# Optimization experiments

Measured on AMD Instinct MI355X. Metric: run time of the kernel, lower is better.

## Reference

```python
import jax, jax.numpy as jnp
import numpy as np

BATCH, SEQ, STATE, OBS, INP = 4096, 512, 16, 8, 4


def setup_inputs() -> dict:
    key = jax.random.key(0)
    ks = jax.random.split(key, 5)
    # scale A to spectral radius ~0.3 so the 512-step recursion is stable
    A = jax.random.normal(ks[0], (STATE, STATE), jnp.float32) * (0.3 / np.sqrt(STATE))
    B = jax.random.normal(ks[1], (STATE, INP), jnp.float32) * 0.1
    C = jax.random.normal(ks[2], (OBS, STATE), jnp.float32) * (1.0 / np.sqrt(STATE))
    Q = jnp.eye(STATE, dtype=jnp.float32)   # module default when Q is None
    R = jnp.eye(OBS, dtype=jnp.float32)     # module default when R is None
    x0 = jnp.zeros((STATE,), jnp.float32)   # module default initial_state_mean
    obs = jax.random.normal(ks[3], (BATCH, SEQ, OBS), jnp.float32)
    u = jax.random.normal(ks[4], (BATCH, SEQ, INP), jnp.float32)
    return {"obs": obs, "u": u, "A": A, "B": B, "C": C, "Q": Q, "R": R, "x0": x0}


def reference(obs, u, A, B, C, Q, R, x0):
    Bsz = obs.shape[0]
    S = A.shape[0]
    eyeS = jnp.eye(S, dtype=obs.dtype)
    x_init = jnp.broadcast_to(x0, (Bsz, S))                 # (B,S), P0 = I per module init
    P_init = jnp.broadcast_to(eyeS, (Bsz, S, S))

    def step(carry, inp):
        x, P = carry                                        # x:(B,S)  P:(B,S,S)
        u_k, z_k = inp                                      # (B,I), (B,O)
        # stage 1: prediction
        x_prior = x @ A.T + u_k @ B.T                       # (B,S)
        P_prior = A @ P @ A.T + Q                           # (B,S,S)
        # stage 2: measurement update
        Smat = C @ P_prior @ C.T + R                        # (B,O,O) innovation covariance
        K = P_prior @ C.T @ jnp.linalg.inv(Smat)            # (B,S,O)
        innov = z_k - x_prior @ C.T                         # (B,O)
        x_post = x_prior + jnp.einsum('bso,bo->bs', K, innov)
        P_post = (eyeS - K @ C) @ P_prior                   # (B,S,S)
        return (x_post, P_post), x_post

    inp_seq = (jnp.swapaxes(u, 0, 1), jnp.swapaxes(obs, 0, 1))  # time-major for scan
    _, xs = jax.lax.scan(step, (x_init, P_init), inp_seq)       # xs: (T,B,S)
    return jnp.swapaxes(xs, 0, 1)                               # (B,T,S) == states_est[:,1:,:]
```

## Files before the change

### kernel.cpp

```cpp
#include <hip/hip_runtime.h>
#include <hip/hip_bf16.h>

#define SEQ   512
#define BATCH 4096
#define NS    16
#define NO    8
#define NI    4
#define NK    12
#define CH    32
#define CL    (SEQ/CH)
#define CW    16

__device__ __align__(16) float g_gains[NK * 448];
__device__ int   g_isf32_data;
__device__ float g_x0[NS];

static __device__ __forceinline__ float bf2f_us(unsigned short v) {
    unsigned int u = ((unsigned int)v) << 16;
    return __uint_as_float(u);
}

static __device__ __forceinline__ float4 ld4(const float* p) { return *(const float4*)p; }
static __device__ __forceinline__ void st4(float* p, float4 v) { *(float4*)p = v; }
static __device__ __forceinline__ void fma4(float4& a, float s, float4 b) {
    a.x += s*b.x; a.y += s*b.y; a.z += s*b.z; a.w += s*b.w;
}
static __device__ __forceinline__ void fnma4(float4& a, float s, float4 b) {
    a.x -= s*b.x; a.y -= s*b.y; a.z -= s*b.z; a.w -= s*b.w;
}

__global__ __launch_bounds__(64) void riccati_kernel(
        const void* __restrict__ Ap, const void* __restrict__ Bp,
        const void* __restrict__ Cp, const void* __restrict__ Qp,
        const void* __restrict__ Rp, const void* __restrict__ x0p,
        const void* __restrict__ obsp) {
    __shared__ __align__(16) float A[NS*NS], AT[NS*NS], Q[NS*NS];
    __shared__ __align__(16) float P[NS*NS], AP[NS*NS], Pp[NS*NS];
    __shared__ __align__(16) float Cm[NO*NS], CT[NS*NO], Bm[NS*NI], R[NO*NO];
    __shared__ __align__(16) float CA[NO*NS], CB[NO*NI];
    __shared__ __align__(16) float CP[NO*NS], PCt[NS*NO], K[NS*NO];
    __shared__ __align__(16) float G[NO*2*NO];
    __shared__ int sflag_p, sflag_d;

    const int t  = threadIdx.x;
    const int i  = t >> 2;
    const int jq = t & 3;
    const int j0 = jq * 4;

    if (t == 0) { sflag_p = 0; sflag_d = 0; }
    __syncthreads();
    {
        const unsigned short* ah = (const unsigned short*)Ap;
        for (int s = 0; s < 4; ++s) {
            float v = fabsf(bf2f_us(ah[t + 64*s]));
            if (!(v < 16.0f)) sflag_p = 1;
        }
        const unsigned short* oh = (const unsigned short*)obsp;
        for (int s = 0; s < 32; ++s) {
            float w = fabsf(bf2f_us(oh[t + 64*s]));
            if (!(w < 16.0f)) sflag_d = 1;
        }
    }
    __syncthreads();
    const bool f32p = (sflag_p != 0);
    if (t == 0) g_isf32_data = (sflag_d != 0) ? 1 : 0;

    auto ld = [&](const void* p, int idx) -> float {
        return f32p ? ((const float*)p)[idx]
                    : bf2f_us(((const unsigned short*)p)[idx]);
    };

    for (int q = t; q < NS*NS; q += 64) {
        A[q] = ld(Ap, q);
        Q[q] = ld(Qp, q);
        P[q] = ((q >> 4) == (q & 15)) ? 1.0f : 0.0f;
    }
    Bm[t] = ld(Bp, t);
    for (int q = t; q < NO*NS; q += 64) Cm[q] = ld(Cp, q);
    R[t] = ld(Rp, t);
    if (t < NS) g_x0[t] = ld(x0p, t);
    __syncthreads();

    for (int q = t; q < NS*NS; q += 64) AT[(q & 15)*NS + (q >> 4)] = A[q];
    for (int q = t; q < NO*NS; q += 64) CT[(q & 15)*NO + (q >> 4)] = Cm[q];
    if (t < 32) {
        const int io = t >> 2;
        float4 acc = make_float4(0.f, 0.f, 0.f, 0.f);
        for (int l = 0; l < NS; ++l) fma4(acc, Cm[io*NS + l], ld4(&A[l*NS + j0]));
        st4(&CA[io*NS + j0], acc);
    } else if (t < 40) {
        const int io = t - 32;
        float4 acc = make_float4(0.f, 0.f, 0.f, 0.f);
        for (int l = 0; l < NS; ++l) fma4(acc, Cm[io*NS + l], ld4(&Bm[l*NI]));
        st4(&CB[io*NI], acc);
    }
    __syncthreads();

    for (int k = 0; k < NK; ++k) {
        {
            float4 acc = make_float4(0.f, 0.f, 0.f, 0.f);
            for (int l = 0; l < NS; ++l) fma4(acc, A[i*NS + l], ld4(&P[l*NS + j0]));
            st4(&AP[i*NS + j0], acc);
        }
        __syncthreads();
        {
            float4 acc = ld4(&Q[i*NS + j0]);
            for (int l = 0; l < NS; ++l) fma4(acc, AP[i*NS + l], ld4(&AT[l*NS + j0]));
            st4(&Pp[i*NS + j0], acc);
        }
        __syncthreads();
        if (t < 32) {
            const int io = t >> 2;
            float4 acc = make_float4(0.f, 0.f, 0.f, 0.f);
            for (int l = 0; l < NS; ++l) fma4(acc, Cm[io*NS + l], ld4(&Pp[l*NS + j0]));
            st4(&CP[io*NS + j0], acc);
        } else {
            const int t2 = t - 32;
            const int i2 = t2 >> 1, jb = (t2 & 1) * 4;
            float4 acc = make_float4(0.f, 0.f, 0.f, 0.f);
            for (int l = 0; l < NS; ++l) fma4(acc, Pp[i2*NS + l], ld4(&CT[l*NO + jb]));
            st4(&PCt[i2*NO + jb], acc);
        }
        __syncthreads();
        if (t < 32) {
            const int io = t >> 2;
            if (jq < 2) {
                float4 acc = ld4(&R[io*NO + j0]);
                for (int l = 0; l < NS; ++l) fma4(acc, CP[io*NS + l], ld4(&CT[l*NO + j0]));
                st4(&G[io*2*NO + j0], acc);
            } else {
                float4 v = make_float4((j0 + 0 - NO) == io ? 1.f : 0.f,
                                       (j0 + 1 - NO) == io ? 1.f : 0.f,
                                       (j0 + 2 - NO) == io ? 1.f : 0.f,
                                       (j0 + 3 - NO) == io ? 1.f : 0.f);
                st4(&G[io*2*NO + j0], v);
            }
        }
        __syncthreads();
        for (int p = 0; p < NO; ++p) {
            float piv = 1.f, gip = 0.f;
            float4 gp4 = make_float4(0.f, 0.f, 0.f, 0.f);
            float4 g4  = make_float4(0.f, 0.f, 0.f, 0.f);
            if (t < 32) {
                const int io = t >> 2;
                piv = G[p*2*NO + p];
                gip = G[io*2*NO + p];
                gp4 = ld4(&G[p*2*NO + j0]);
                g4  = ld4(&G[io*2*NO + j0]);
            }
            __syncthreads();
            if (t < 32) {
                const int io = t >> 2;
                const float inv = 1.0f / piv;
                float4 r4 = make_float4(gp4.x*inv, gp4.y*inv, gp4.z*inv, gp4.w*inv);
                float4 w;
                if (io == p) w = r4;
                else w = make_float4(g4.x - gip*r4.x, g4.y - gip*r4.y,
                                     g4.z - gip*r4.z, g4.w - gip*r4.w);
                st4(&G[io*2*NO + j0], w);
            }
            __syncthreads();
        }
        if (t < 32) {
            const int i2 = t >> 1, jb = (t & 1) * 4;
            float4 acc = make_float4(0.f, 0.f, 0.f, 0.f);
            for (int l = 0; l < NO; ++l) fma4(acc, PCt[i2*NO + l], ld4(&G[l*2*NO + NO + jb]));
            st4(&K[i2*NO + jb], acc);
        }
        __syncthreads();
        float* outp = g_gains + k * 448;
        {
            float4 m4 = ld4(&A[i*NS + j0]);
            float4 pn = ld4(&Pp[i*NS + j0]);
            for (int l = 0; l < NO; ++l) {
                const float kk = K[i*NO + l];
                fnma4(m4, kk, ld4(&CA[l*NS + j0]));
                fnma4(pn, kk, ld4(&CP[l*NS + j0]));
            }
            st4(outp + i*NS + j0, m4);
            st4(&P[i*NS + j0], pn);
        }
        if (jq == 0) {
            float4 n4 = ld4(&Bm[i*NI]);
            for (int l = 0; l < NO; ++l) fnma4(n4, K[i*NO + l], ld4(&CB[l*NI]));
            st4(outp + 256 + i*NI, n4);
        } else if (jq < 3) {
            const int jb = (jq - 1) * 4;
            st4(outp + 320 + i*NO + jb, ld4(&K[i*NO + jb]));
        }
        __syncthreads();
    }
}

template<bool F32>
static __device__ __forceinline__ void run_filter(
        const void* __restrict__ obsv, const void* __restrict__ uv,
        float* __restrict__ out, int c, int b, const float* __restrict__ sg) {
    const int cL = c * CL;
    const int k0 = (c == 0) ? 0 : (cL - CW);
    const int kend = cL + CL;

    float x[NS];
#pragma unroll
    for (int s = 0; s < NS; ++s) x[s] = (c == 0) ? g_x0[s] : 0.0f;
    float xp[NS];

    float* op = out + (size_t)b * SEQ * NS;

    const float*          upf = (const float*)uv   + (size_t)b * SEQ * NI;
    const float*          zpf = (const float*)obsv + (size_t)b * SEQ * NO;
    const unsigned short* upb = (const unsigned short*)uv   + (size_t)b * SEQ * NI;
    const unsigned short* zpb = (const unsigned short*)obsv + (size_t)b * SEQ * NO;

    float4 uf, zf0, zf1;
    uint2 ub; uint4 zb;
    if (F32) {
        uf  = *(const float4*)(upf + (size_t)k0 * NI);
        zf0 = *(const float4*)(zpf + (size_t)k0 * NO);
        zf1 = *(const float4*)(zpf + (size_t)k0 * NO + 4);
    } else {
        ub = *(const uint2*)(upb + (size_t)k0 * NI);
        zb = *(const uint4*)(zpb + (size_t)k0 * NO);
    }

    for (int k = k0; k < kend; ++k) {
        float uu[NI], zz[NO];
        if (F32) {
            uu[0]=uf.x; uu[1]=uf.y; uu[2]=uf.z; uu[3]=uf.w;
            zz[0]=zf0.x; zz[1]=zf0.y; zz[2]=zf0.z; zz[3]=zf0.w;
            zz[4]=zf1.x; zz[5]=zf1.y; zz[6]=zf1.z; zz[7]=zf1.w;
            if (k + 1 < kend) {
                uf  = *(const float4*)(upf + (size_t)(k+1) * NI);
                zf0 = *(const float4*)(zpf + (size_t)(k+1) * NO);
                zf1 = *(const float4*)(zpf + (size_t)(k+1) * NO + 4);
            }
        } else {
            const uint2 uc = ub; const uint4 zc = zb;
            if (k + 1 < kend) {
                ub = *(const uint2*)(upb + (size_t)(k+1) * NI);
                zb = *(const uint4*)(zpb + (size_t)(k+1) * NO);
            }
            uu[0] = bf2f_us(uc.x & 0xffffu); uu[1] = bf2f_us(uc.x >> 16);
            uu[2] = bf2f_us(uc.y & 0xffffu); uu[3] = bf2f_us(uc.y >> 16);
            zz[0] = bf2f_us(zc.x & 0xffffu); zz[1] = bf2f_us(zc.x >> 16);
            zz[2] = bf2f_us(zc.y & 0xffffu); zz[3] = bf2f_us(zc.y >> 16);
            zz[4] = bf2f_us(zc.z & 0xffffu); zz[5] = bf2f_us(zc.z >> 16);
            zz[6] = bf2f_us(zc.w & 0xffffu); zz[7] = bf2f_us(zc.w >> 16);
        }

        const int idx = (k < NK) ? k : (NK - 1);
        const float4* G = (const float4*)sg + idx * 112;

        float xn[NS];
#pragma unroll
        for (int r = 0; r < NS; ++r) {
            float4 m0 = G[r*4 + 0], m1 = G[r*4 + 1], m2 = G[r*4 + 2], m3 = G[r*4 + 3];
            float acc;
            acc  = m0.x*x[0]  + m0.y*x[1]  + m0.z*x[2]  + m0.w*x[3];
            acc += m1.x*x[4]  + m1.y*x[5]  + m1.z*x[6]  + m1.w*x[7];
            acc += m2.x*x[8]  + m2.y*x[9]  + m2.z*x[10] + m2.w*x[11];
            acc += m3.x*x[12] + m3.y*x[13] + m3.z*x[14] + m3.w*x[15];
            float4 nv = G[64 + r];
            acc += nv.x*uu[0] + nv.y*uu[1] + nv.z*uu[2] + nv.w*uu[3];
            float4 k0v = G[80 + r*2], k1v = G[80 + r*2 + 1];
            acc += k0v.x*zz[0] + k0v.y*zz[1] + k0v.z*zz[2] + k0v.w*zz[3];
            acc += k1v.x*zz[4] + k1v.y*zz[5] + k1v.z*zz[6] + k1v.w*zz[7];
            xn[r] = acc;
        }
#pragma unroll
        for (int r = 0; r < NS; ++r) x[r] = xn[r];

        if (k >= cL) {
            if (((k - cL) & 1) == 0) {
#pragma unroll
                for (int r = 0; r < NS; ++r) xp[r] = x[r];
            } else {
                float4* dst = (float4*)(op + (size_t)(k - 1) * NS);
                dst[0] = make_float4(xp[0],  xp[1],  xp[2],  xp[3]);
                dst[1] = make_float4(xp[4],  xp[5],  xp[6],  xp[7]);
                dst[2] = make_float4(xp[8],  xp[9],  xp[10], xp[11]);
                dst[3] = make_float4(xp[12], xp[13], xp[14], xp[15]);
                dst[4] = make_float4(x[0],   x[1],   x[2],   x[3]);
                dst[5] = make_float4(x[4],   x[5],   x[6],   x[7]);
                dst[6] = make_float4(x[8],   x[9],   x[10],  x[11]);
                dst[7] = make_float4(x[12],  x[13],  x[14],  x[15]);
            }
        }
    }
}

__global__ __launch_bounds__(256) void filter_kernel(
        const void* __restrict__ obs, const void* __restrict__ u,
        float* __restrict__ out) {
    __shared__ __align__(16) float sg[NK * 448];
    for (int q = threadIdx.x; q < NK * 112; q += 256)
        ((float4*)sg)[q] = ((const float4*)g_gains)[q];
    __syncthreads();

    const int c  = blockIdx.x / (BATCH/256);
    const int bg = blockIdx.x % (BATCH/256);
    const int b  = bg * 256 + threadIdx.x;
    if (g_isf32_data) run_filter<true >(obs, u, out, c, b, sg);
    else              run_filter<false>(obs, u, out, c, b, sg);
}

extern "C" void kernel_launch(void* const* d_in, const int* in_sizes, int n_in,
                              void* d_out, int out_size, void* d_ws, size_t ws_size,
                              hipStream_t stream) {
    const void* obs = d_in[0];
    const void* u   = d_in[1];
    const void* A   = d_in[2];
    const void* B   = d_in[3];
    const void* C   = d_in[4];
    const void* Q   = d_in[5];
    const void* R   = d_in[6];
    const void* x0  = d_in[7];
    float* out = (float*)d_out;

    riccati_kernel<<<1, 64, 0, stream>>>(A, B, C, Q, R, x0, obs);
    filter_kernel<<<dim3(CH * (BATCH/256)), dim3(256), 0, stream>>>(obs, u, out);
}
```

Before: 349.8 us.

## Split each batch element's state across four lanes with DPP broadcast and register gains

The filter now assigns four lanes per batch element, each owning four state rows. Each lane keeps its slice of the gain matrices in registers instead of reading them from shared memory, and the full state is rebuilt every step with DPP quad broadcasts. The time-chunk count is halved so there is less warm-up overlap, and the loop is unrolled by two with double-buffered input loads. In exchange, every lane loads the same u/z inputs, and there are DPP cross-lane operations plus more register pressure from the held gains.

```diff
diff --git a/kernel.cpp b/kernel.cpp
--- a/kernel.cpp
+++ b/kernel.cpp
@@ -7,13 +7,13 @@
 #define NO    8
 #define NI    4
 #define NK    12
-#define CH    32
+#define CH    16
 #define CL    (SEQ/CH)
 #define CW    16
 
 __device__ __align__(16) float g_gains[NK * 448];
 __device__ int   g_isf32_data;
-__device__ float g_x0[NS];
+__device__ __align__(16) float g_x0[NS];
 
 static __device__ __forceinline__ float bf2f_us(unsigned short v) {
     unsigned int u = ((unsigned int)v) << 16;
@@ -192,54 +192,108 @@
     }
 }
 
+
+template<int S>
+static __device__ __forceinline__ float qb(float v) {
+    return __int_as_float(__builtin_amdgcn_mov_dpp(__float_as_int(v), S*0x55, 0xF, 0xF, true));
+}
+
+struct Gains { float4 m[4][4]; float4 n[4]; float4 kv[4][2]; };
+
+static __device__ __forceinline__ void load_gains(const float* __restrict__ gb,
+                                                  int q, Gains& G) {
+#pragma unroll
+    for (int rr = 0; rr < 4; ++rr) {
+        const int row = q*4 + rr;
+        const float* rowp = gb + row*16;
+#pragma unroll
+        for (int cq = 0; cq < 4; ++cq) G.m[rr][cq] = ld4(rowp + cq*4);
+        G.n[rr]     = ld4(gb + 256 + row*4);
+        G.kv[rr][0] = ld4(gb + 320 + row*8);
+        G.kv[rr][1] = ld4(gb + 320 + row*8 + 4);
+    }
+}
+
+static __device__ __forceinline__ void step(const Gains& G, float xq[4],
+                                            const float uu[4], const float zz[8]) {
+    float xf[16];
+#pragma unroll
+    for (int r = 0; r < 4; ++r) {
+        xf[0*4+r] = qb<0>(xq[r]);
+        xf[1*4+r] = qb<1>(xq[r]);
+        xf[2*4+r] = qb<2>(xq[r]);
+        xf[3*4+r] = qb<3>(xq[r]);
+    }
+#pragma unroll
+    for (int rr = 0; rr < 4; ++rr) {
+        float acc;
+        acc  = G.m[rr][0].x*xf[0]  + G.m[rr][0].y*xf[1]  + G.m[rr][0].z*xf[2]  + G.m[rr][0].w*xf[3];
+        acc += G.m[rr][1].x*xf[4]  + G.m[rr][1].y*xf[5]  + G.m[rr][1].z*xf[6]  + G.m[rr][1].w*xf[7];
+        acc += G.m[rr][2].x*xf[8]  + G.m[rr][2].y*xf[9]  + G.m[rr][2].z*xf[10] + G.m[rr][2].w*xf[11];
+        acc += G.m[rr][3].x*xf[12] + G.m[rr][3].y*xf[13] + G.m[rr][3].z*xf[14] + G.m[rr][3].w*xf[15];
+        acc += G.n[rr].x*uu[0] + G.n[rr].y*uu[1] + G.n[rr].z*uu[2] + G.n[rr].w*uu[3];
+        acc += G.kv[rr][0].x*zz[0] + G.kv[rr][0].y*zz[1] + G.kv[rr][0].z*zz[2] + G.kv[rr][0].w*zz[3];
+        acc += G.kv[rr][1].x*zz[4] + G.kv[rr][1].y*zz[5] + G.kv[rr][1].z*zz[6] + G.kv[rr][1].w*zz[7];
+        xq[rr] = acc;
+    }
+}
+
 template<bool F32>
-static __device__ __forceinline__ void run_filter(
-        const void* __restrict__ obsv, const void* __restrict__ uv,
-        float* __restrict__ out, int c, int b, const float* __restrict__ sg) {
-    const int cL = c * CL;
-    const int k0 = (c == 0) ? 0 : (cL - CW);
+static __device__ __forceinline__ void run4(const void* __restrict__ obsv,
+        const void* __restrict__ uv, float* __restrict__ out,
+        int c, int b, int q) {
+    const int cL   = c * CL;
+    const int k0   = (c == 0) ? 0 : (cL - CW);
     const int kend = cL + CL;
 
-    float x[NS];
-#pragma unroll
-    for (int s = 0; s < NS; ++s) x[s] = (c == 0) ? g_x0[s] : 0.0f;
-    float xp[NS];
-
-    float* op = out + (size_t)b * SEQ * NS;
-
-    const float*          upf = (const float*)uv   + (size_t)b * SEQ * NI;
-    const float*          zpf = (const float*)obsv + (size_t)b * SEQ * NO;
-    const unsigned short* upb = (const unsigned short*)uv   + (size_t)b * SEQ * NI;
-    const unsigned short* zpb = (const unsigned short*)obsv + (size_t)b * SEQ * NO;
-
-    float4 uf, zf0, zf1;
-    uint2 ub; uint4 zb;
+    Gains G;
+    float xq[4];
+    if (c == 0) {
+#pragma unroll
+        for (int r = 0; r < 4; ++r) xq[r] = g_x0[q*4 + r];
+        load_gains(g_gains, q, G);
+    } else {
+#pragma unroll
+        for (int r = 0; r < 4; ++r) xq[r] = 0.0f;
+        load_gains(g_gains + (NK-1)*448, q, G);
+    }
+
+    float* op = out + (size_t)b * (SEQ*NS) + q*4;
+
+    const float* upf = (const float*)uv   + (size_t)b * SEQ * NI;
+    const float* zpf = (const float*)obsv + (size_t)b * SEQ * NO;
+    const uint2* upb = (const uint2*)uv   + (size_t)b * SEQ;
+    const uint4* zpb = (const uint4*)obsv + (size_t)b * SEQ;
+
+    float4 uA, uB, zA0, zA1, zB0, zB1;
+    uint2 ubA, ubB; uint4 zbA, zbB;
     if (F32) {
-        uf  = *(const float4*)(upf + (size_t)k0 * NI);
-        zf0 = *(const float4*)(zpf + (size_t)k0 * NO);
-        zf1 = *(const float4*)(zpf + (size_t)k0 * NO + 4);
+        uA  = ld4(upf + (size_t)k0*NI);
+        zA0 = ld4(zpf + (size_t)k0*NO); zA1 = ld4(zpf + (size_t)k0*NO + 4);
+        uB  = ld4(upf + (size_t)(k0+1)*NI);
+        zB0 = ld4(zpf + (size_t)(k0+1)*NO); zB1 = ld4(zpf + (size_t)(k0+1)*NO + 4);
     } else {
-        ub = *(const uint2*)(upb + (size_t)k0 * NI);
-        zb = *(const uint4*)(zpb + (size_t)k0 * NO);
-    }
-
-    for (int k = k0; k < kend; ++k) {
-        float uu[NI], zz[NO];
+        ubA = upb[k0];   zbA = zpb[k0];
+        ubB = upb[k0+1]; zbB = zpb[k0+1];
+    }
+
+    const bool vary = (c == 0);
+    float xe[4];
+
+    for (int k = k0; k < kend; k += 2) {
+        float uu[4], zz[8];
         if (F32) {
-            uu[0]=uf.x; uu[1]=uf.y; uu[2]=uf.z; uu[3]=uf.w;
-            zz[0]=zf0.x; zz[1]=zf0.y; zz[2]=zf0.z; zz[3]=zf0.w;
-            zz[4]=zf1.x; zz[5]=zf1.y; zz[6]=zf1.z; zz[7]=zf1.w;
-            if (k + 1 < kend) {
-                uf  = *(const float4*)(upf + (size_t)(k+1) * NI);
-                zf0 = *(const float4*)(zpf + (size_t)(k+1) * NO);
-                zf1 = *(const float4*)(zpf + (size_t)(k+1) * NO + 4);
+            uu[0]=uA.x; uu[1]=uA.y; uu[2]=uA.z; uu[3]=uA.w;
+            zz[0]=zA0.x; zz[1]=zA0.y; zz[2]=zA0.z; zz[3]=zA0.w;
+            zz[4]=zA1.x; zz[5]=zA1.y; zz[6]=zA1.z; zz[7]=zA1.w;
+            if (k + 2 < kend) {
+                uA  = ld4(upf + (size_t)(k+2)*NI);
+                zA0 = ld4(zpf + (size_t)(k+2)*NO);
+                zA1 = ld4(zpf + (size_t)(k+2)*NO + 4);
             }
         } else {
-            const uint2 uc = ub; const uint4 zc = zb;
-            if (k + 1 < kend) {
-                ub = *(const uint2*)(upb + (size_t)(k+1) * NI);
-                zb = *(const uint4*)(zpb + (size_t)(k+1) * NO);
-            }
+            const uint2 uc = ubA; const uint4 zc = zbA;
+            if (k + 2 < kend) { ubA = upb[k+2]; zbA = zpb[k+2]; }
             uu[0] = bf2f_us(uc.x & 0xffffu); uu[1] = bf2f_us(uc.x >> 16);
             uu[2] = bf2f_us(uc.y & 0xffffu); uu[3] = bf2f_us(uc.y >> 16);
             zz[0] = bf2f_us(zc.x & 0xffffu); zz[1] = bf2f_us(zc.x >> 16);
@@ -247,61 +301,50 @@
             zz[4] = bf2f_us(zc.z & 0xffffu); zz[5] = bf2f_us(zc.z >> 16);
             zz[6] = bf2f_us(zc.w & 0xffffu); zz[7] = bf2f_us(zc.w >> 16);
         }
-
-        const int idx = (k < NK) ? k : (NK - 1);
-        const float4* G = (const float4*)sg + idx * 112;
-
-        float xn[NS];
-#pragma unroll
-        for (int r = 0; r < NS; ++r) {
-            float4 m0 = G[r*4 + 0], m1 = G[r*4 + 1], m2 = G[r*4 + 2], m3 = G[r*4 + 3];
-            float acc;
-            acc  = m0.x*x[0]  + m0.y*x[1]  + m0.z*x[2]  + m0.w*x[3];
-            acc += m1.x*x[4]  + m1.y*x[5]  + m1.z*x[6]  + m1.w*x[7];
-            acc += m2.x*x[8]  + m2.y*x[9]  + m2.z*x[10] + m2.w*x[11];
-            acc += m3.x*x[12] + m3.y*x[13] + m3.z*x[14] + m3.w*x[15];
-            float4 nv = G[64 + r];
-            acc += nv.x*uu[0] + nv.y*uu[1] + nv.z*uu[2] + nv.w*uu[3];
-            float4 k0v = G[80 + r*2], k1v = G[80 + r*2 + 1];
-            acc += k0v.x*zz[0] + k0v.y*zz[1] + k0v.z*zz[2] + k0v.w*zz[3];
-            acc += k1v.x*zz[4] + k1v.y*zz[5] + k1v.z*zz[6] + k1v.w*zz[7];
-            xn[r] = acc;
-        }
-#pragma unroll
-        for (int r = 0; r < NS; ++r) x[r] = xn[r];
+        if (vary && k >= 1 && k < NK) load_gains(g_gains + (size_t)k*448, q, G);
+        step(G, xq, uu, zz);
+#pragma unroll
+        for (int r = 0; r < 4; ++r) xe[r] = xq[r];
+
+        if (F32) {
+            uu[0]=uB.x; uu[1]=uB.y; uu[2]=uB.z; uu[3]=uB.w;
+            zz[0]=zB0.x; zz[1]=zB0.y; zz[2]=zB0.z; zz[3]=zB0.w;
+            zz[4]=zB1.x; zz[5]=zB1.y; zz[6]=zB1.z; zz[7]=zB1.w;
+            if (k + 3 < kend) {
+                uB  = ld4(upf + (size_t)(k+3)*NI);
+                zB0 = ld4(zpf + (size_t)(k+3)*NO);
+                zB1 = ld4(zpf + (size_t)(k+3)*NO + 4);
+            }
+        } else {
+            const uint2 uc = ubB; const uint4 zc = zbB;
+            if (k + 3 < kend) { ubB = upb[k+3]; zbB = zpb[k+3]; }
+            uu[0] = bf2f_us(uc.x & 0xffffu); uu[1] = bf2f_us(uc.x >> 16);
+            uu[2] = bf2f_us(uc.y & 0xffffu); uu[3] = bf2f_us(uc.y >> 16);
+            zz[0] = bf2f_us(zc.x & 0xffffu); zz[1] = bf2f_us(zc.x >> 16);
+            zz[2] = bf2f_us(zc.y & 0xffffu); zz[3] = bf2f_us(zc.y >> 16);
+            zz[4] = bf2f_us(zc.z & 0xffffu); zz[5] = bf2f_us(zc.z >> 16);
+            zz[6] = bf2f_us(zc.w & 0xffffu); zz[7] = bf2f_us(zc.w >> 16);
+        }
+        if (vary && (k+1) < NK) load_gains(g_gains + (size_t)(k+1)*448, q, G);
+        step(G, xq, uu, zz);
 
         if (k >= cL) {
-            if (((k - cL) & 1) == 0) {
-#pragma unroll
-                for (int r = 0; r < NS; ++r) xp[r] = x[r];
-            } else {
-                float4* dst = (float4*)(op + (size_t)(k - 1) * NS);
-                dst[0] = make_float4(xp[0],  xp[1],  xp[2],  xp[3]);
-                dst[1] = make_float4(xp[4],  xp[5],  xp[6],  xp[7]);
-                dst[2] = make_float4(xp[8],  xp[9],  xp[10], xp[11]);
-                dst[3] = make_float4(xp[12], xp[13], xp[14], xp[15]);
-                dst[4] = make_float4(x[0],   x[1],   x[2],   x[3]);
-                dst[5] = make_float4(x[4],   x[5],   x[6],   x[7]);
-                dst[6] = make_float4(x[8],   x[9],   x[10],  x[11]);
-                dst[7] = make_float4(x[12],  x[13],  x[14],  x[15]);
-            }
-        }
-    }
-}
-
-__global__ __launch_bounds__(256) void filter_kernel(
+            st4(op + (size_t)k*NS,     make_float4(xe[0], xe[1], xe[2], xe[3]));
+            st4(op + (size_t)(k+1)*NS, make_float4(xq[0], xq[1], xq[2], xq[3]));
+        }
+    }
+}
+
+__global__ __launch_bounds__(256, 2) void filter_kernel(
         const void* __restrict__ obs, const void* __restrict__ u,
         float* __restrict__ out) {
-    __shared__ __align__(16) float sg[NK * 448];
-    for (int q = threadIdx.x; q < NK * 112; q += 256)
-        ((float4*)sg)[q] = ((const float4*)g_gains)[q];
-    __syncthreads();
-
-    const int c  = blockIdx.x / (BATCH/256);
-    const int bg = blockIdx.x % (BATCH/256);
-    const int b  = bg * 256 + threadIdx.x;
-    if (g_isf32_data) run_filter<true >(obs, u, out, c, b, sg);
-    else              run_filter<false>(obs, u, out, c, b, sg);
+    const int c  = blockIdx.x >> 6;
+    const int eg = blockIdx.x & 63;
+    const int g  = threadIdx.x >> 2;
+    const int q  = threadIdx.x & 3;
+    const int b  = eg * 64 + g;
+    if (g_isf32_data) run4<true >(obs, u, out, c, b, q);
+    else              run4<false>(obs, u, out, c, b, q);
 }
 
 extern "C" void kernel_launch(void* const* d_in, const int* in_sizes, int n_in,
@@ -318,5 +361,5 @@
     float* out = (float*)d_out;
 
     riccati_kernel<<<1, 64, 0, stream>>>(A, B, C, Q, R, x0, obs);
-    filter_kernel<<<dim3(CH * (BATCH/256)), dim3(256), 0, stream>>>(obs, u, out);
-}
+    filter_kernel<<<dim3(CH * 64), dim3(256), 0, stream>>>(obs, u, out);
+}
```

After: 1.375 ms. 293% more time.

## Read gains from global memory, specialize chunk-0 path, unroll filter loop by two

Applied to the files above, without the earlier changes.

Removes the shared-memory staging of the gain tables and the block-wide barrier. Filter steps now read gains straight from global memory, where the uniform addresses let the compiler use scalar loads. A compile-time C0 template flag gives non-first chunks a fixed steady-state gain pointer. The time loop is unrolled by two with double-buffered input prefetch, replacing the per-step parity branch for output stores. This trades LDS reads for scalar/constant-cache loads and removes the sync, at some register-pressure risk.

```diff
diff --git a/kernel.cpp b/kernel.cpp
--- a/kernel.cpp
+++ b/kernel.cpp
@@ -13,7 +13,7 @@
 
 __device__ __align__(16) float g_gains[NK * 448];
 __device__ int   g_isf32_data;
-__device__ float g_x0[NS];
+__device__ __align__(16) float g_x0[NS];
 
 static __device__ __forceinline__ float bf2f_us(unsigned short v) {
     unsigned int u = ((unsigned int)v) << 16;
@@ -192,18 +192,42 @@
     }
 }
 
-template<bool F32>
+
+static __device__ __forceinline__ void step_mem(const float* __restrict__ g,
+        float x[NS], const float uu[NI], const float zz[NO]) {
+    const float4* G = (const float4*)g;
+    float xn[NS];
+#pragma unroll
+    for (int r = 0; r < NS; ++r) {
+        float4 m0 = G[r*4 + 0], m1 = G[r*4 + 1], m2 = G[r*4 + 2], m3 = G[r*4 + 3];
+        float acc;
+        acc  = m0.x*x[0]  + m0.y*x[1]  + m0.z*x[2]  + m0.w*x[3];
+        acc += m1.x*x[4]  + m1.y*x[5]  + m1.z*x[6]  + m1.w*x[7];
+        acc += m2.x*x[8]  + m2.y*x[9]  + m2.z*x[10] + m2.w*x[11];
+        acc += m3.x*x[12] + m3.y*x[13] + m3.z*x[14] + m3.w*x[15];
+        float4 nv = G[64 + r];
+        acc += nv.x*uu[0] + nv.y*uu[1] + nv.z*uu[2] + nv.w*uu[3];
+        float4 k0v = G[80 + r*2], k1v = G[80 + r*2 + 1];
+        acc += k0v.x*zz[0] + k0v.y*zz[1] + k0v.z*zz[2] + k0v.w*zz[3];
+        acc += k1v.x*zz[4] + k1v.y*zz[5] + k1v.z*zz[6] + k1v.w*zz[7];
+        xn[r] = acc;
+    }
+#pragma unroll
+    for (int r = 0; r < NS; ++r) x[r] = xn[r];
+}
+
+template<bool F32, bool C0>
 static __device__ __forceinline__ void run_filter(
         const void* __restrict__ obsv, const void* __restrict__ uv,
-        float* __restrict__ out, int c, int b, const float* __restrict__ sg) {
-    const int cL = c * CL;
-    const int k0 = (c == 0) ? 0 : (cL - CW);
+        float* __restrict__ out, int c, int b) {
+    const int cL   = c * CL;
+    const int k0   = C0 ? 0 : (cL - CW);
     const int kend = cL + CL;
 
     float x[NS];
 #pragma unroll
-    for (int s = 0; s < NS; ++s) x[s] = (c == 0) ? g_x0[s] : 0.0f;
-    float xp[NS];
+    for (int s = 0; s < NS; ++s) x[s] = C0 ? g_x0[s] : 0.0f;
+    float xe[NS];
 
     float* op = out + (size_t)b * SEQ * NS;
 
@@ -212,33 +236,38 @@
     const unsigned short* upb = (const unsigned short*)uv   + (size_t)b * SEQ * NI;
     const unsigned short* zpb = (const unsigned short*)obsv + (size_t)b * SEQ * NO;
 
-    float4 uf, zf0, zf1;
-    uint2 ub; uint4 zb;
+    float4 uA, uB, zA0, zA1, zB0, zB1;
+    uint2 ubA, ubB; uint4 zbA, zbB;
     if (F32) {
-        uf  = *(const float4*)(upf + (size_t)k0 * NI);
-        zf0 = *(const float4*)(zpf + (size_t)k0 * NO);
-        zf1 = *(const float4*)(zpf + (size_t)k0 * NO + 4);
+        uA  = ld4(upf + (size_t)k0*NI);
+        zA0 = ld4(zpf + (size_t)k0*NO); zA1 = ld4(zpf + (size_t)k0*NO + 4);
+        uB  = ld4(upf + (size_t)(k0+1)*NI);
+        zB0 = ld4(zpf + (size_t)(k0+1)*NO); zB1 = ld4(zpf + (size_t)(k0+1)*NO + 4);
     } else {
-        ub = *(const uint2*)(upb + (size_t)k0 * NI);
-        zb = *(const uint4*)(zpb + (size_t)k0 * NO);
-    }
-
-    for (int k = k0; k < kend; ++k) {
+        ubA = *(const uint2*)(upb + (size_t)k0*NI);
+        zbA = *(const uint4*)(zpb + (size_t)k0*NO);
+        ubB = *(const uint2*)(upb + (size_t)(k0+1)*NI);
+        zbB = *(const uint4*)(zpb + (size_t)(k0+1)*NO);
+    }
+
+    const float* __restrict__ gsteady = g_gains + (size_t)(NK-1) * 448;
+
+    for (int k = k0; k < kend; k += 2) {
         float uu[NI], zz[NO];
         if (F32) {
-            uu[0]=uf.x; uu[1]=uf.y; uu[2]=uf.z; uu[3]=uf.w;
-            zz[0]=zf0.x; zz[1]=zf0.y; zz[2]=zf0.z; zz[3]=zf0.w;
-            zz[4]=zf1.x; zz[5]=zf1.y; zz[6]=zf1.z; zz[7]=zf1.w;
-            if (k + 1 < kend) {
-                uf  = *(const float4*)(upf + (size_t)(k+1) * NI);
-                zf0 = *(const float4*)(zpf + (size_t)(k+1) * NO);
-                zf1 = *(const float4*)(zpf + (size_t)(k+1) * NO + 4);
+            uu[0]=uA.x; uu[1]=uA.y; uu[2]=uA.z; uu[3]=uA.w;
+            zz[0]=zA0.x; zz[1]=zA0.y; zz[2]=zA0.z; zz[3]=zA0.w;
+            zz[4]=zA1.x; zz[5]=zA1.y; zz[6]=zA1.z; zz[7]=zA1.w;
+            if (k + 2 < kend) {
+                uA  = ld4(upf + (size_t)(k+2)*NI);
+                zA0 = ld4(zpf + (size_t)(k+2)*NO);
+                zA1 = ld4(zpf + (size_t)(k+2)*NO + 4);
             }
         } else {
-            const uint2 uc = ub; const uint4 zc = zb;
-            if (k + 1 < kend) {
-                ub = *(const uint2*)(upb + (size_t)(k+1) * NI);
-                zb = *(const uint4*)(zpb + (size_t)(k+1) * NO);
+            const uint2 uc = ubA; const uint4 zc = zbA;
+            if (k + 2 < kend) {
+                ubA = *(const uint2*)(upb + (size_t)(k+2)*NI);
+                zbA = *(const uint4*)(zpb + (size_t)(k+2)*NO);
             }
             uu[0] = bf2f_us(uc.x & 0xffffu); uu[1] = bf2f_us(uc.x >> 16);
             uu[2] = bf2f_us(uc.y & 0xffffu); uu[3] = bf2f_us(uc.y >> 16);
@@ -247,44 +276,52 @@
             zz[4] = bf2f_us(zc.z & 0xffffu); zz[5] = bf2f_us(zc.z >> 16);
             zz[6] = bf2f_us(zc.w & 0xffffu); zz[7] = bf2f_us(zc.w >> 16);
         }
-
-        const int idx = (k < NK) ? k : (NK - 1);
-        const float4* G = (const float4*)sg + idx * 112;
-
-        float xn[NS];
+        {
+            const float* gp = C0 ? (g_gains + (size_t)((k < NK) ? k : (NK-1)) * 448)
+                                 : gsteady;
+            step_mem(gp, x, uu, zz);
+        }
 #pragma unroll
-        for (int r = 0; r < NS; ++r) {
-            float4 m0 = G[r*4 + 0], m1 = G[r*4 + 1], m2 = G[r*4 + 2], m3 = G[r*4 + 3];
-            float acc;
-            acc  = m0.x*x[0]  + m0.y*x[1]  + m0.z*x[2]  + m0.w*x[3];
-            acc += m1.x*x[4]  + m1.y*x[5]  + m1.z*x[6]  + m1.w*x[7];
-            acc += m2.x*x[8]  + m2.y*x[9]  + m2.z*x[10] + m2.w*x[11];
-            acc += m3.x*x[12] + m3.y*x[13] + m3.z*x[14] + m3.w*x[15];
-            float4 nv = G[64 + r];
-            acc += nv.x*uu[0] + nv.y*uu[1] + nv.z*uu[2] + nv.w*uu[3];
-            float4 k0v = G[80 + r*2], k1v = G[80 + r*2 + 1];
-            acc += k0v.x*zz[0] + k0v.y*zz[1] + k0v.z*zz[2] + k0v.w*zz[3];
-            acc += k1v.x*zz[4] + k1v.y*zz[5] + k1v.z*zz[6] + k1v.w*zz[7];
-            xn[r] = acc;
-        }
-#pragma unroll
-        for (int r = 0; r < NS; ++r) x[r] = xn[r];
+        for (int r = 0; r < NS; ++r) xe[r] = x[r];
+
+        if (F32) {
+            uu[0]=uB.x; uu[1]=uB.y; uu[2]=uB.z; uu[3]=uB.w;
+            zz[0]=zB0.x; zz[1]=zB0.y; zz[2]=zB0.z; zz[3]=zB0.w;
+            zz[4]=zB1.x; zz[5]=zB1.y; zz[6]=zB1.z; zz[7]=zB1.w;
+            if (k + 3 < kend) {
+                uB  = ld4(upf + (size_t)(k+3)*NI);
+                zB0 = ld4(zpf + (size_t)(k+3)*NO);
+                zB1 = ld4(zpf + (size_t)(k+3)*NO + 4);
+            }
+        } else {
+            const uint2 uc = ubB; const uint4 zc = zbB;
+            if (k + 3 < kend) {
+                ubB = *(const uint2*)(upb + (size_t)(k+3)*NI);
+                zbB = *(const uint4*)(zpb + (size_t)(k+3)*NO);
+            }
+            uu[0] = bf2f_us(uc.x & 0xffffu); uu[1] = bf2f_us(uc.x >> 16);
+            uu[2] = bf2f_us(uc.y & 0xffffu); uu[3] = bf2f_us(uc.y >> 16);
+            zz[0] = bf2f_us(zc.x & 0xffffu); zz[1] = bf2f_us(zc.x >> 16);
+            zz[2] = bf2f_us(zc.y & 0xffffu); zz[3] = bf2f_us(zc.y >> 16);
+            zz[4] = bf2f_us(zc.z & 0xffffu); zz[5] = bf2f_us(zc.z >> 16);
+            zz[6] = bf2f_us(zc.w & 0xffffu); zz[7] = bf2f_us(zc.w >> 16);
+        }
+        {
+            const float* gp = C0 ? (g_gains + (size_t)(((k+1) < NK) ? (k+1) : (NK-1)) * 448)
+                                 : gsteady;
+            step_mem(gp, x, uu, zz);
+        }
 
         if (k >= cL) {
-            if (((k - cL) & 1) == 0) {
-#pragma unroll
-                for (int r = 0; r < NS; ++r) xp[r] = x[r];
-            } else {
-                float4* dst = (float4*)(op + (size_t)(k - 1) * NS);
-                dst[0] = make_float4(xp[0],  xp[1],  xp[2],  xp[3]);
-                dst[1] = make_float4(xp[4],  xp[5],  xp[6],  xp[7]);
-                dst[2] = make_float4(xp[8],  xp[9],  xp[10], xp[11]);
-                dst[3] = make_float4(xp[12], xp[13], xp[14], xp[15]);
-                dst[4] = make_float4(x[0],   x[1],   x[2],   x[3]);
-                dst[5] = make_float4(x[4],   x[5],   x[6],   x[7]);
-                dst[6] = make_float4(x[8],   x[9],   x[10],  x[11]);
-                dst[7] = make_float4(x[12],  x[13],  x[14],  x[15]);
-            }
+            float4* dst = (float4*)(op + (size_t)k * NS);
+            dst[0] = make_float4(xe[0],  xe[1],  xe[2],  xe[3]);
+            dst[1] = make_float4(xe[4],  xe[5],  xe[6],  xe[7]);
+            dst[2] = make_float4(xe[8],  xe[9],  xe[10], xe[11]);
+            dst[3] = make_float4(xe[12], xe[13], xe[14], xe[15]);
+            dst[4] = make_float4(x[0],   x[1],   x[2],   x[3]);
+            dst[5] = make_float4(x[4],   x[5],   x[6],   x[7]);
+            dst[6] = make_float4(x[8],   x[9],   x[10],  x[11]);
+            dst[7] = make_float4(x[12],  x[13],  x[14],  x[15]);
         }
     }
 }
@@ -292,16 +329,16 @@
 __global__ __launch_bounds__(256) void filter_kernel(
         const void* __restrict__ obs, const void* __restrict__ u,
         float* __restrict__ out) {
-    __shared__ __align__(16) float sg[NK * 448];
-    for (int q = threadIdx.x; q < NK * 112; q += 256)
-        ((float4*)sg)[q] = ((const float4*)g_gains)[q];
-    __syncthreads();
-
-    const int c  = blockIdx.x / (BATCH/256);
-    const int bg = blockIdx.x % (BATCH/256);
-    const int b  = bg * 256 + threadIdx.x;
-    if (g_isf32_data) run_filter<true >(obs, u, out, c, b, sg);
-    else              run_filter<false>(obs, u, out, c, b, sg);
+    const int c  = blockIdx.x >> 4;
+    const int eg = blockIdx.x & 15;
+    const int b  = eg * 256 + threadIdx.x;
+    if (g_isf32_data) {
+        if (c == 0) run_filter<true, true >(obs, u, out, c, b);
+        else        run_filter<true, false>(obs, u, out, c, b);
+    } else {
+        if (c == 0) run_filter<false, true >(obs, u, out, c, b);
+        else        run_filter<false, false>(obs, u, out, c, b);
+    }
 }
 
 extern "C" void kernel_launch(void* const* d_in, const int* in_sizes, int n_in,
@@ -318,5 +355,5 @@
     float* out = (float*)d_out;
 
     riccati_kernel<<<1, 64, 0, stream>>>(A, B, C, Q, R, x0, obs);
-    filter_kernel<<<dim3(CH * (BATCH/256)), dim3(256), 0, stream>>>(obs, u, out);
-}
+    filter_kernel<<<dim3(CH * 16), dim3(256), 0, stream>>>(obs, u, out);
+}
```

After: 369.0 us. 5.5% more time.

## Run the steady-state filter recurrence on MFMA with split-fp16 precision emulation

Applied to the files above, without the earlier changes.

Replaces the per-thread scalar 16x28 matrix-vector update with 16x16x16 fp16 MFMA instructions. Each wavefront handles 64 batch elements as four 16-column tiles. The fp32 gains, state and inputs are split into hi/lo fp16 pairs, and three MFMAs per product approximate fp32 accuracy. The chunk count drops from 32 to 16, so fewer warm-up steps are spent on redundant overlap, and the gains are held in registers instead of shared memory. The cost is six MFMAs per step plus the split conversions. The state also now makes a serial round trip between the MFMA accumulators and the fp16 splits every step, which adds latency on the dependency chain.

```diff
diff --git a/kernel.cpp b/kernel.cpp
--- a/kernel.cpp
+++ b/kernel.cpp
@@ -7,13 +7,16 @@
 #define NO    8
 #define NI    4
 #define NK    12
-#define CH    32
+#define CH    16
 #define CL    (SEQ/CH)
 #define CW    16
 
 __device__ __align__(16) float g_gains[NK * 448];
 __device__ int   g_isf32_data;
-__device__ float g_x0[NS];
+__device__ __align__(16) float g_x0[NS];
+
+typedef __attribute__((ext_vector_type(4))) _Float16 h4;
+typedef __attribute__((ext_vector_type(4))) float    f4;
 
 static __device__ __forceinline__ float bf2f_us(unsigned short v) {
     unsigned int u = ((unsigned int)v) << 16;
@@ -192,98 +195,133 @@
     }
 }
 
-template<bool F32>
-static __device__ __forceinline__ void run_filter(
+
+static __device__ __forceinline__ void split4(float a, float b, float c, float d,
+                                              h4& hi, h4& lo) {
+    _Float16 ha = (_Float16)a, hb = (_Float16)b, hc = (_Float16)c, hd = (_Float16)d;
+    hi = (h4){ha, hb, hc, hd};
+    lo = (h4){(_Float16)(a - (float)ha), (_Float16)(b - (float)hb),
+              (_Float16)(c - (float)hc), (_Float16)(d - (float)hd)};
+}
+
+struct AF { h4 mh, ml, ah, al; };
+
+static __device__ __forceinline__ void load_af(const float* __restrict__ gb,
+                                               int row, int g, AF& F) {
+    float4 m = ld4(gb + row*NS + g*4);
+    split4(m.x, m.y, m.z, m.w, F.mh, F.ml);
+    float4 a;
+    if      (g == 0) a = ld4(gb + 256 + row*NI);
+    else if (g == 1) a = ld4(gb + 320 + row*NO);
+    else if (g == 2) a = ld4(gb + 320 + row*NO + 4);
+    else             a = make_float4(0.f, 0.f, 0.f, 0.f);
+    split4(a.x, a.y, a.z, a.w, F.ah, F.al);
+}
+
+static __device__ __forceinline__ f4 stept(const AF& F, f4 X,
+                                           float i0, float i1, float i2, float i3) {
+    h4 xh, xl, bh, bl;
+    split4(X.x, X.y, X.z, X.w, xh, xl);
+    split4(i0, i1, i2, i3, bh, bl);
+    f4 acc = {0.f, 0.f, 0.f, 0.f};
+    acc = __builtin_amdgcn_mfma_f32_16x16x16f16(F.mh, xh, acc, 0, 0, 0);
+    acc = __builtin_amdgcn_mfma_f32_16x16x16f16(F.mh, xl, acc, 0, 0, 0);
+    acc = __builtin_amdgcn_mfma_f32_16x16x16f16(F.ml, xh, acc, 0, 0, 0);
+    acc = __builtin_amdgcn_mfma_f32_16x16x16f16(F.ah, bh, acc, 0, 0, 0);
+    acc = __builtin_amdgcn_mfma_f32_16x16x16f16(F.ah, bl, acc, 0, 0, 0);
+    acc = __builtin_amdgcn_mfma_f32_16x16x16f16(F.al, bh, acc, 0, 0, 0);
+    return acc;
+}
+
+static __device__ __forceinline__ float4 up2(uint2 v) {
+    return make_float4(bf2f_us(v.x & 0xffffu), bf2f_us(v.x >> 16),
+                       bf2f_us(v.y & 0xffffu), bf2f_us(v.y >> 16));
+}
+
+template<bool F32, bool C0>
+static __device__ __forceinline__ void run_mfma(
         const void* __restrict__ obsv, const void* __restrict__ uv,
-        float* __restrict__ out, int c, int b, const float* __restrict__ sg) {
-    const int cL = c * CL;
-    const int k0 = (c == 0) ? 0 : (cL - CW);
-    const int kend = cL + CL;
-
-    float x[NS];
-#pragma unroll
-    for (int s = 0; s < NS; ++s) x[s] = (c == 0) ? g_x0[s] : 0.0f;
-    float xp[NS];
-
-    float* op = out + (size_t)b * SEQ * NS;
-
-    const float*          upf = (const float*)uv   + (size_t)b * SEQ * NI;
-    const float*          zpf = (const float*)obsv + (size_t)b * SEQ * NO;
-    const unsigned short* upb = (const unsigned short*)uv   + (size_t)b * SEQ * NI;
-    const unsigned short* zpb = (const unsigned short*)obsv + (size_t)b * SEQ * NO;
-
-    float4 uf, zf0, zf1;
-    uint2 ub; uint4 zb;
+        float* __restrict__ out, int c, int eb) {
+    const int lane = threadIdx.x & 63;
+    const int n = lane & 15, g = lane >> 4;
+    const int cL = c * CL, k0 = C0 ? 0 : (cL - CW), kend = cL + CL;
+
+    AF F;
+    load_af(C0 ? g_gains : (g_gains + (NK-1)*448), n, g, F);
+
+    f4 X0, X1, X2, X3;
+    if (C0) {
+        float4 xi = ld4(&g_x0[g*4]);
+        X0 = (f4){xi.x, xi.y, xi.z, xi.w}; X1 = X0; X2 = X0; X3 = X0;
+    } else {
+        X0 = (f4){0.f, 0.f, 0.f, 0.f};     X1 = X0; X2 = X0; X3 = X0;
+    }
+
+    const int e0 = eb + n, e1 = e0 + 16, e2 = e0 + 32, e3 = e0 + 48;
+    float* o0 = out + (size_t)e0 * SEQ * NS + g*4;
+    float* o1 = out + (size_t)e1 * SEQ * NS + g*4;
+    float* o2 = out + (size_t)e2 * SEQ * NS + g*4;
+    float* o3 = out + (size_t)e3 * SEQ * NS + g*4;
+
+    const int st = (g == 0) ? NI : NO;
+    const bool z3 = (g == 3);
+
     if (F32) {
-        uf  = *(const float4*)(upf + (size_t)k0 * NI);
-        zf0 = *(const float4*)(zpf + (size_t)k0 * NO);
-        zf1 = *(const float4*)(zpf + (size_t)k0 * NO + 4);
+        auto mk = [&](int e) {
+            return (g == 0) ? ((const float*)uv   + ((size_t)e*SEQ + k0)*NI)
+                            : ((const float*)obsv + ((size_t)e*SEQ + k0)*NO + ((g >= 2) ? 4 : 0));
+        };
+        const float *p0 = mk(e0), *p1 = mk(e1), *p2 = mk(e2), *p3 = mk(e3);
+        float4 c0 = ld4(p0), c1 = ld4(p1), c2 = ld4(p2), c3 = ld4(p3);
+        float4 d0 = ld4(p0+st), d1 = ld4(p1+st), d2 = ld4(p2+st), d3 = ld4(p3+st);
+        for (int k = k0; k < kend; ++k) {
+            float4 v0 = c0, v1 = c1, v2 = c2, v3 = c3;
+            c0 = d0; c1 = d1; c2 = d2; c3 = d3;
+            if (k + 2 < kend) {
+                d0 = ld4(p0 + 2*st); d1 = ld4(p1 + 2*st);
+                d2 = ld4(p2 + 2*st); d3 = ld4(p3 + 2*st);
+            }
+            p0 += st; p1 += st; p2 += st; p3 += st;
+            X0 = stept(F, X0, z3?0.f:v0.x, z3?0.f:v0.y, z3?0.f:v0.z, z3?0.f:v0.w);
+            X1 = stept(F, X1, z3?0.f:v1.x, z3?0.f:v1.y, z3?0.f:v1.z, z3?0.f:v1.w);
+            X2 = stept(F, X2, z3?0.f:v2.x, z3?0.f:v2.y, z3?0.f:v2.z, z3?0.f:v2.w);
+            X3 = stept(F, X3, z3?0.f:v3.x, z3?0.f:v3.y, z3?0.f:v3.z, z3?0.f:v3.w);
+            if (C0 && (k + 1) < NK) load_af(g_gains + (size_t)(k+1)*448, n, g, F);
+            if (k >= cL) {
+                *(f4*)(o0 + (size_t)k * NS) = X0;
+                *(f4*)(o1 + (size_t)k * NS) = X1;
+                *(f4*)(o2 + (size_t)k * NS) = X2;
+                *(f4*)(o3 + (size_t)k * NS) = X3;
+            }
+        }
     } else {
-        ub = *(const uint2*)(upb + (size_t)k0 * NI);
-        zb = *(const uint4*)(zpb + (size_t)k0 * NO);
-    }
-
-    for (int k = k0; k < kend; ++k) {
-        float uu[NI], zz[NO];
-        if (F32) {
-            uu[0]=uf.x; uu[1]=uf.y; uu[2]=uf.z; uu[3]=uf.w;
-            zz[0]=zf0.x; zz[1]=zf0.y; zz[2]=zf0.z; zz[3]=zf0.w;
-            zz[4]=zf1.x; zz[5]=zf1.y; zz[6]=zf1.z; zz[7]=zf1.w;
-            if (k + 1 < kend) {
-                uf  = *(const float4*)(upf + (size_t)(k+1) * NI);
-                zf0 = *(const float4*)(zpf + (size_t)(k+1) * NO);
-                zf1 = *(const float4*)(zpf + (size_t)(k+1) * NO + 4);
-            }
-        } else {
-            const uint2 uc = ub; const uint4 zc = zb;
-            if (k + 1 < kend) {
-                ub = *(const uint2*)(upb + (size_t)(k+1) * NI);
-                zb = *(const uint4*)(zpb + (size_t)(k+1) * NO);
-            }
-            uu[0] = bf2f_us(uc.x & 0xffffu); uu[1] = bf2f_us(uc.x >> 16);
-            uu[2] = bf2f_us(uc.y & 0xffffu); uu[3] = bf2f_us(uc.y >> 16);
-            zz[0] = bf2f_us(zc.x & 0xffffu); zz[1] = bf2f_us(zc.x >> 16);
-            zz[2] = bf2f_us(zc.y & 0xffffu); zz[3] = bf2f_us(zc.y >> 16);
-            zz[4] = bf2f_us(zc.z & 0xffffu); zz[5] = bf2f_us(zc.z >> 16);
-            zz[6] = bf2f_us(zc.w & 0xffffu); zz[7] = bf2f_us(zc.w >> 16);
-        }
-
-        const int idx = (k < NK) ? k : (NK - 1);
-        const float4* G = (const float4*)sg + idx * 112;
-
-        float xn[NS];
-#pragma unroll
-        for (int r = 0; r < NS; ++r) {
-            float4 m0 = G[r*4 + 0], m1 = G[r*4 + 1], m2 = G[r*4 + 2], m3 = G[r*4 + 3];
-            float acc;
-            acc  = m0.x*x[0]  + m0.y*x[1]  + m0.z*x[2]  + m0.w*x[3];
-            acc += m1.x*x[4]  + m1.y*x[5]  + m1.z*x[6]  + m1.w*x[7];
-            acc += m2.x*x[8]  + m2.y*x[9]  + m2.z*x[10] + m2.w*x[11];
-            acc += m3.x*x[12] + m3.y*x[13] + m3.z*x[14] + m3.w*x[15];
-            float4 nv = G[64 + r];
-            acc += nv.x*uu[0] + nv.y*uu[1] + nv.z*uu[2] + nv.w*uu[3];
-            float4 k0v = G[80 + r*2], k1v = G[80 + r*2 + 1];
-            acc += k0v.x*zz[0] + k0v.y*zz[1] + k0v.z*zz[2] + k0v.w*zz[3];
-            acc += k1v.x*zz[4] + k1v.y*zz[5] + k1v.z*zz[6] + k1v.w*zz[7];
-            xn[r] = acc;
-        }
-#pragma unroll
-        for (int r = 0; r < NS; ++r) x[r] = xn[r];
-
-        if (k >= cL) {
-            if (((k - cL) & 1) == 0) {
-#pragma unroll
-                for (int r = 0; r < NS; ++r) xp[r] = x[r];
-            } else {
-                float4* dst = (float4*)(op + (size_t)(k - 1) * NS);
-                dst[0] = make_float4(xp[0],  xp[1],  xp[2],  xp[3]);
-                dst[1] = make_float4(xp[4],  xp[5],  xp[6],  xp[7]);
-                dst[2] = make_float4(xp[8],  xp[9],  xp[10], xp[11]);
-                dst[3] = make_float4(xp[12], xp[13], xp[14], xp[15]);
-                dst[4] = make_float4(x[0],   x[1],   x[2],   x[3]);
-                dst[5] = make_float4(x[4],   x[5],   x[6],   x[7]);
-                dst[6] = make_float4(x[8],   x[9],   x[10],  x[11]);
-                dst[7] = make_float4(x[12],  x[13],  x[14],  x[15]);
+        auto mk = [&](int e) {
+            return (g == 0) ? ((const unsigned short*)uv   + ((size_t)e*SEQ + k0)*NI)
+                            : ((const unsigned short*)obsv + ((size_t)e*SEQ + k0)*NO + ((g >= 2) ? 4 : 0));
+        };
+        const unsigned short *p0 = mk(e0), *p1 = mk(e1), *p2 = mk(e2), *p3 = mk(e3);
+        uint2 c0 = *(const uint2*)p0, c1 = *(const uint2*)p1,
+              c2 = *(const uint2*)p2, c3 = *(const uint2*)p3;
+        uint2 d0 = *(const uint2*)(p0+st), d1 = *(const uint2*)(p1+st),
+              d2 = *(const uint2*)(p2+st), d3 = *(const uint2*)(p3+st);
+        for (int k = k0; k < kend; ++k) {
+            float4 v0 = up2(c0), v1 = up2(c1), v2 = up2(c2), v3 = up2(c3);
+            c0 = d0; c1 = d1; c2 = d2; c3 = d3;
+            if (k + 2 < kend) {
+                d0 = *(const uint2*)(p0 + 2*st); d1 = *(const uint2*)(p1 + 2*st);
+                d2 = *(const uint2*)(p2 + 2*st); d3 = *(const uint2*)(p3 + 2*st);
+            }
+            p0 += st; p1 += st; p2 += st; p3 += st;
+            X0 = stept(F, X0, z3?0.f:v0.x, z3?0.f:v0.y, z3?0.f:v0.z, z3?0.f:v0.w);
+            X1 = stept(F, X1, z3?0.f:v1.x, z3?0.f:v1.y, z3?0.f:v1.z, z3?0.f:v1.w);
+            X2 = stept(F, X2, z3?0.f:v2.x, z3?0.f:v2.y, z3?0.f:v2.z, z3?0.f:v2.w);
+            X3 = stept(F, X3, z3?0.f:v3.x, z3?0.f:v3.y, z3?0.f:v3.z, z3?0.f:v3.w);
+            if (C0 && (k + 1) < NK) load_af(g_gains + (size_t)(k+1)*448, n, g, F);
+            if (k >= cL) {
+                *(f4*)(o0 + (size_t)k * NS) = X0;
+                *(f4*)(o1 + (size_t)k * NS) = X1;
+                *(f4*)(o2 + (size_t)k * NS) = X2;
+                *(f4*)(o3 + (size_t)k * NS) = X3;
             }
         }
     }
@@ -292,16 +330,17 @@
 __global__ __launch_bounds__(256) void filter_kernel(
         const void* __restrict__ obs, const void* __restrict__ u,
         float* __restrict__ out) {
-    __shared__ __align__(16) float sg[NK * 448];
-    for (int q = threadIdx.x; q < NK * 112; q += 256)
-        ((float4*)sg)[q] = ((const float4*)g_gains)[q];
-    __syncthreads();
-
-    const int c  = blockIdx.x / (BATCH/256);
-    const int bg = blockIdx.x % (BATCH/256);
-    const int b  = bg * 256 + threadIdx.x;
-    if (g_isf32_data) run_filter<true >(obs, u, out, c, b, sg);
-    else              run_filter<false>(obs, u, out, c, b, sg);
+    const int c  = blockIdx.x >> 4;
+    const int eg = blockIdx.x & 15;
+    const int w  = threadIdx.x >> 6;
+    const int eb = eg * 256 + w * 64;
+    if (g_isf32_data) {
+        if (c == 0) run_mfma<true,  true >(obs, u, out, c, eb);
+        else        run_mfma<true,  false>(obs, u, out, c, eb);
+    } else {
+        if (c == 0) run_mfma<false, true >(obs, u, out, c, eb);
+        else        run_mfma<false, false>(obs, u, out, c, eb);
+    }
 }
 
 extern "C" void kernel_launch(void* const* d_in, const int* in_sizes, int n_in,
@@ -318,5 +357,5 @@
     float* out = (float*)d_out;
 
     riccati_kernel<<<1, 64, 0, stream>>>(A, B, C, Q, R, x0, obs);
-    filter_kernel<<<dim3(CH * (BATCH/256)), dim3(256), 0, stream>>>(obs, u, out);
-}
+    filter_kernel<<<dim3(CH * 16), dim3(256), 0, stream>>>(obs, u, out);
+}
```

Measured after the change: 334.6 us. 4.4% less time.
